# Optimization experiments

Measured on AMD Instinct MI355X. Metric: run time of the kernel, lower is better.

The kernel has to match this reference:

```python
import jax, jax.numpy as jnp
import numpy as np

D_MODEL = 1024
N_HEADS = 16
D_K = 64
D_V = 64
B = 2
S = 2048
NEG = -1e9
EPS = 1e-5  # torch nn.LayerNorm default


def setup_inputs() -> dict:
    key = jax.random.key(0)
    ks = jax.random.split(key, 8)
    inp = {
        "input_Q": jax.random.normal(ks[0], (B, S, D_MODEL), jnp.float32),
        "input_K": jax.random.normal(ks[1], (B, S, D_MODEL), jnp.float32),
        "input_V": jax.random.normal(ks[2], (B, S, D_MODEL), jnp.float32),
        "attn_mask": jax.random.randint(ks[3], (B, S, S), 0, 2).astype(bool),
        # torch nn.Linear weights are [out_features, in_features]; scale like default init
        "W_Q": jax.random.normal(ks[4], (N_HEADS * D_K, D_MODEL), jnp.float32) * (1.0 / np.sqrt(D_MODEL)),
        "W_K": jax.random.normal(ks[5], (N_HEADS * D_K, D_MODEL), jnp.float32) * (1.0 / np.sqrt(D_MODEL)),
        "W_V": jax.random.normal(ks[6], (N_HEADS * D_V, D_MODEL), jnp.float32) * (1.0 / np.sqrt(D_MODEL)),
        "W_fc": jax.random.normal(ks[7], (D_MODEL, N_HEADS * D_V), jnp.float32) * (1.0 / np.sqrt(N_HEADS * D_V)),
    }
    return inp


def _layernorm(x):
    # fresh nn.LayerNorm(d_model): weight=1, bias=0
    mu = jnp.mean(x, axis=-1, keepdims=True)
    var = jnp.mean(jnp.square(x - mu), axis=-1, keepdims=True)
    return (x - mu) * jax.lax.rsqrt(var + EPS)


def reference(input_Q, input_K, input_V, attn_mask, W_Q, W_K, W_V, W_fc):
    residual = input_Q
    # projections: x @ W.T, then split heads -> [B, H, S, d]
    def split_heads(x, d):
        return x.reshape(B, S, N_HEADS, d).transpose(0, 2, 1, 3)

    Q = split_heads(input_Q @ W_Q.T, D_K)
    K = split_heads(input_K @ W_K.T, D_K)
    V = split_heads(input_V @ W_V.T, D_V)

    scores = jnp.einsum("bhqd,bhkd->bhqk", Q, K) / np.sqrt(D_K).astype(np.float32)
    scores = jnp.where(attn_mask[:, None, :, :], NEG, scores)
    attn = jax.nn.softmax(scores, axis=-1)
    context = jnp.einsum("bhqk,bhkd->bhqd", attn, V)  # [B,H,S,Dv]
    context = context.transpose(0, 2, 1, 3).reshape(B, S, N_HEADS * D_V)
    output = context @ W_fc.T
    return _layernorm(output + residual), attn
```

## Files before the change

kernel.cpp:

```cpp
#include <hip/hip_runtime.h>

#define NB 2
#define SS 2048
#define DMODEL 1024
#define NH 16
#define DHEAD 64
#define QSCALE 0.1803368867f

typedef __bf16 bf16;
typedef bf16 bf16x8 __attribute__((ext_vector_type(8)));
typedef float f32x4 __attribute__((ext_vector_type(4)));
typedef unsigned char u8;

static __device__ __forceinline__ f32x4 mfma_16x16x32(bf16x8 a, bf16x8 b, f32x4 c) {
    return __builtin_amdgcn_mfma_f32_16x16x32_bf16(a, b, c, 0, 0, 0);
}

static __device__ __forceinline__ float fast_exp2(float x) {
#if __has_builtin(__builtin_amdgcn_exp2f)
    return __builtin_amdgcn_exp2f(x);
#else
    return __expf(x * 0.6931471805599453f);
#endif
}

static __device__ __forceinline__ bf16x8 cvt8(float4 u, float4 v) {
    bf16x8 r;
    r[0]=(bf16)u.x; r[1]=(bf16)u.y; r[2]=(bf16)u.z; r[3]=(bf16)u.w;
    r[4]=(bf16)v.x; r[5]=(bf16)v.y; r[6]=(bf16)v.z; r[7]=(bf16)v.w;
    return r;
}

__global__ __launch_bounds__(256) void pack_mask(const int* __restrict__ m,
                                                 u8* __restrict__ mb, int n4)
{
    const int i = blockIdx.x * blockDim.x + threadIdx.x;
    if (i < n4) {
        const int4 v = ((const int4*)m)[i];
        uchar4 o;
        o.x = (u8)v.x; o.y = (u8)v.y; o.z = (u8)v.z; o.w = (u8)v.w;
        ((uchar4*)mb)[i] = o;
    }
}

__global__ __launch_bounds__(256) void cvt_pair(const float* __restrict__ s0, bf16* __restrict__ d0, int n0_8,
                                                const float* __restrict__ s1, bf16* __restrict__ d1, int n1_8)
{
    const int i = blockIdx.x * blockDim.x + threadIdx.x;
    if (i < n0_8) {
        float4 u = ((const float4*)s0)[(size_t)i * 2];
        float4 v = ((const float4*)s0)[(size_t)i * 2 + 1];
        ((bf16x8*)d0)[i] = cvt8(u, v);
    } else if (i < n0_8 + n1_8) {
        const int j = i - n0_8;
        float4 u = ((const float4*)s1)[(size_t)j * 2];
        float4 v = ((const float4*)s1)[(size_t)j * 2 + 1];
        ((bf16x8*)d1)[j] = cvt8(u, v);
    }
}

__global__ __launch_bounds__(256) void gemm_bt(const bf16* __restrict__ A,
                                               const bf16* __restrict__ W,
                                               void* __restrict__ out, int mode,
                                               float scale)
{
    __shared__ bf16 As[128][40];
    __shared__ bf16 Ws[128][40];

    const int t  = threadIdx.x;
    const int wv = t >> 6, ln = t & 63, lo = ln & 15, qd = ln >> 4;
    const int wm = wv >> 1, wn = wv & 1;

    const int flat = blockIdx.x;
    const int swz  = ((flat & 7) << 5) + (flat >> 3);
    const int m0   = (swz >> 3) << 7;
    const int n0   = (swz & 7) << 7;

    const int srow = t >> 2, scol = (t & 3) << 3;
    const bf16* ap = A + (size_t)(m0 + srow) * DMODEL + scol;
    const bf16* wp = W + (size_t)(n0 + srow) * DMODEL + scol;

    f32x4 acc[4][4];
    #pragma unroll
    for (int i = 0; i < 4; ++i)
        #pragma unroll
        for (int j = 0; j < 4; ++j) acc[i][j] = (f32x4){0.f,0.f,0.f,0.f};

    bf16x8 a0 = *(const bf16x8*)ap;
    bf16x8 a1 = *(const bf16x8*)(ap + (size_t)64 * DMODEL);
    bf16x8 w0 = *(const bf16x8*)wp;
    bf16x8 w1 = *(const bf16x8*)(wp + (size_t)64 * DMODEL);

    for (int k0 = 0; k0 < DMODEL; k0 += 32) {
        __syncthreads();
        *(bf16x8*)&As[srow][scol]      = a0;
        *(bf16x8*)&As[64 + srow][scol] = a1;
        *(bf16x8*)&Ws[srow][scol]      = w0;
        *(bf16x8*)&Ws[64 + srow][scol] = w1;
        if (k0 + 32 < DMODEL) {
            a0 = *(const bf16x8*)(ap + k0 + 32);
            a1 = *(const bf16x8*)(ap + (size_t)64 * DMODEL + k0 + 32);
            w0 = *(const bf16x8*)(wp + k0 + 32);
            w1 = *(const bf16x8*)(wp + (size_t)64 * DMODEL + k0 + 32);
        }
        __syncthreads();
        bf16x8 af[4], wf[4];
        #pragma unroll
        for (int i = 0; i < 4; ++i)
            af[i] = *(const bf16x8*)&As[(wm << 6) + (i << 4) + lo][qd << 3];
        #pragma unroll
        for (int j = 0; j < 4; ++j)
            wf[j] = *(const bf16x8*)&Ws[(wn << 6) + (j << 4) + lo][qd << 3];
        #pragma unroll
        for (int i = 0; i < 4; ++i)
            #pragma unroll
            for (int j = 0; j < 4; ++j)
                acc[i][j] = mfma_16x16x32(af[i], wf[j], acc[i][j]);
    }

    #pragma unroll
    for (int i = 0; i < 4; ++i) {
        #pragma unroll
        for (int j = 0; j < 4; ++j) {
            #pragma unroll
            for (int r = 0; r < 4; ++r) {
                const int m = m0 + (wm << 6) + (i << 4) + (qd << 2) + r;
                const int n = n0 + (wn << 6) + (j << 4) + lo;
                const float v = acc[i][j][r] * scale;
                if (mode == 0) {
                    ((bf16*)out)[(size_t)m * DMODEL + n] = (bf16)v;
                } else if (mode == 1) {
                    ((bf16*)out)[((size_t)(m >> 11) * 1024 + n) * SS + (m & (SS - 1))] = (bf16)v;
                } else {
                    ((float*)out)[(size_t)m * DMODEL + n] = v;
                }
            }
        }
    }
}

__global__ __launch_bounds__(256) void attn_fused(const bf16* __restrict__ Qp,
                                                  const bf16* __restrict__ Kp,
                                                  const bf16* __restrict__ Vt,
                                                  const u8* __restrict__ mb,
                                                  float* __restrict__ attn_out,
                                                  bf16* __restrict__ ctxb)
{
    __shared__ bf16 Ks[2][32][72];
    __shared__ bf16 Pb[4][16][40];

    const int t  = threadIdx.x;
    const int wv = t >> 6, ln = t & 63, lo = ln & 15, qd = ln >> 4;

    const int flat = blockIdx.x;
    const int swz  = ((flat & 7) << 7) + (flat >> 3);
    const int q0 = (swz & 31) << 6;
    const int h  = (swz >> 5) & 15;
    const int b  = swz >> 9;
    const int bh = b * NH + h;

    const bf16* qsrc = Qp + (size_t)(b * SS + q0 + (wv << 4) + lo) * DMODEL + h * DHEAD + (qd << 3);
    const bf16x8 qa0 = *(const bf16x8*)qsrc;
    const bf16x8 qa1 = *(const bf16x8*)(qsrc + 32);

    const int srow = t >> 3, scol = (t & 7) << 3;
    const bf16* kbase = Kp + (size_t)(b * SS + srow) * DMODEL + h * DHEAD + scol;

    const u8* mrp[4];
    #pragma unroll
    for (int r = 0; r < 4; ++r)
        mrp[r] = mb + ((size_t)b * SS + q0 + (wv << 4) + (qd << 2) + r) * SS;

    const bf16* vbase = Vt + ((size_t)bh * DHEAD + lo) * SS + (qd << 3);

    f32x4 o[4];
    float lr[4] = {0.f, 0.f, 0.f, 0.f};
    #pragma unroll
    for (int j = 0; j < 4; ++j) o[j] = (f32x4){0.f,0.f,0.f,0.f};

    bf16x8 kreg = *(const bf16x8*)kbase;
    *(bf16x8*)&Ks[0][srow][scol] = kreg;
    kreg = *(const bf16x8*)(kbase + (size_t)32 * DMODEL);
    __syncthreads();

    for (int c = 0; c < 64; ++c) {
        if (c < 63) {
            *(bf16x8*)&Ks[(c + 1) & 1][srow][scol] = kreg;
            if (c < 62) kreg = *(const bf16x8*)(kbase + (size_t)(c + 2) * 32 * DMODEL);
        }
        const bf16 (*kb)[72] = Ks[c & 1];
        bf16x8 k00 = *(const bf16x8*)&kb[lo][qd << 3];
        bf16x8 k01 = *(const bf16x8*)&kb[lo][32 + (qd << 3)];
        bf16x8 k10 = *(const bf16x8*)&kb[16 + lo][qd << 3];
        bf16x8 k11 = *(const bf16x8*)&kb[16 + lo][32 + (qd << 3)];
        f32x4 s0 = (f32x4){0.f,0.f,0.f,0.f};
        s0 = mfma_16x16x32(qa0, k00, s0);
        s0 = mfma_16x16x32(qa1, k01, s0);
        f32x4 s1 = (f32x4){0.f,0.f,0.f,0.f};
        s1 = mfma_16x16x32(qa0, k10, s1);
        s1 = mfma_16x16x32(qa1, k11, s1);
        const int kc0 = c << 5;
        #pragma unroll
        for (int r = 0; r < 4; ++r) {
            const float e0 = mrp[r][kc0 + lo]      ? 0.f : fast_exp2(s0[r]);
            const float e1 = mrp[r][kc0 + 16 + lo] ? 0.f : fast_exp2(s1[r]);
            lr[r] += e0 + e1;
            Pb[wv][(qd << 2) + r][lo]      = (bf16)e0;
            Pb[wv][(qd << 2) + r][16 + lo] = (bf16)e1;
        }
        bf16x8 pa = *(const bf16x8*)&Pb[wv][lo][qd << 3];
        #pragma unroll
        for (int j = 0; j < 4; ++j) {
            bf16x8 vb = *(const bf16x8*)(vbase + (size_t)(j << 4) * SS + kc0);
            o[j] = mfma_16x16x32(pa, vb, o[j]);
        }
        __syncthreads();
    }

    #pragma unroll
    for (int r = 0; r < 4; ++r) {
        #pragma unroll
        for (int d = 1; d < 16; d <<= 1) lr[r] += __shfl_xor(lr[r], d);
    }
    float Li[4];
    #pragma unroll
    for (int r = 0; r < 4; ++r) Li[r] = 1.f / lr[r];

    #pragma unroll
    for (int j = 0; j < 4; ++j) {
        #pragma unroll
        for (int r = 0; r < 4; ++r) {
            ctxb[(size_t)(b * SS + q0 + (wv << 4) + (qd << 2) + r) * DMODEL
                 + h * DHEAD + (j << 4) + lo] = (bf16)(o[j][r] * Li[r]);
        }
    }

    kreg = *(const bf16x8*)kbase;
    *(bf16x8*)&Ks[0][srow][scol] = kreg;
    kreg = *(const bf16x8*)(kbase + (size_t)32 * DMODEL);
    __syncthreads();

    float* aout = attn_out + ((size_t)bh * SS + q0 + (wv << 4) + (qd << 2)) * SS;

    for (int c = 0; c < 64; ++c) {
        if (c < 63) {
            *(bf16x8*)&Ks[(c + 1) & 1][srow][scol] = kreg;
            if (c < 62) kreg = *(const bf16x8*)(kbase + (size_t)(c + 2) * 32 * DMODEL);
        }
        const bf16 (*kb)[72] = Ks[c & 1];
        bf16x8 k00 = *(const bf16x8*)&kb[lo][qd << 3];
        bf16x8 k01 = *(const bf16x8*)&kb[lo][32 + (qd << 3)];
        bf16x8 k10 = *(const bf16x8*)&kb[16 + lo][qd << 3];
        bf16x8 k11 = *(const bf16x8*)&kb[16 + lo][32 + (qd << 3)];
        f32x4 s0 = (f32x4){0.f,0.f,0.f,0.f};
        s0 = mfma_16x16x32(qa0, k00, s0);
        s0 = mfma_16x16x32(qa1, k01, s0);
        f32x4 s1 = (f32x4){0.f,0.f,0.f,0.f};
        s1 = mfma_16x16x32(qa0, k10, s1);
        s1 = mfma_16x16x32(qa1, k11, s1);
        const int kc0 = c << 5;
        #pragma unroll
        for (int r = 0; r < 4; ++r) {
            const float p0 = mrp[r][kc0 + lo]      ? 0.f : fast_exp2(s0[r]) * Li[r];
            const float p1 = mrp[r][kc0 + 16 + lo] ? 0.f : fast_exp2(s1[r]) * Li[r];
            aout[(size_t)r * SS + kc0 + lo]      = p0;
            aout[(size_t)r * SS + kc0 + 16 + lo] = p1;
        }
        __syncthreads();
    }
}

__global__ __launch_bounds__(256) void ln_resid(const float* __restrict__ O,
                                                const float* __restrict__ resid,
                                                float* __restrict__ out)
{
    const int row = blockIdx.x;
    const int t = threadIdx.x;
    const size_t base = (size_t)row * DMODEL + ((size_t)t << 2);
    const float4 o  = *(const float4*)(O + base);
    const float4 rs = *(const float4*)(resid + base);
    const float x0 = o.x + rs.x, x1 = o.y + rs.y, x2 = o.z + rs.z, x3 = o.w + rs.w;
    float s  = x0 + x1 + x2 + x3;
    float ss = x0*x0 + x1*x1 + x2*x2 + x3*x3;
    #pragma unroll
    for (int d = 32; d > 0; d >>= 1) {
        s  += __shfl_xor(s, d);
        ss += __shfl_xor(ss, d);
    }
    __shared__ float ws1[4], ws2[4];
    if ((t & 63) == 0) { ws1[t >> 6] = s; ws2[t >> 6] = ss; }
    __syncthreads();
    s  = ws1[0] + ws1[1] + ws1[2] + ws1[3];
    ss = ws2[0] + ws2[1] + ws2[2] + ws2[3];
    const float mu  = s * (1.f / DMODEL);
    const float var = ss * (1.f / DMODEL) - mu * mu;
    const float inv = rsqrtf(var + 1e-5f);
    float4 y;
    y.x = (x0 - mu) * inv; y.y = (x1 - mu) * inv;
    y.z = (x2 - mu) * inv; y.w = (x3 - mu) * inv;
    *(float4*)(out + base) = y;
}

extern "C" void kernel_launch(void* const* d_in, const int* in_sizes, int n_in,
                              void* d_out, int out_size, void* d_ws, size_t ws_size,
                              hipStream_t stream)
{
    const float* inQ = (const float*)d_in[0];
    const float* inK = (const float*)d_in[1];
    const float* inV = (const float*)d_in[2];
    const int*   msk = (const int*)d_in[3];
    const float* WQ  = (const float*)d_in[4];
    const float* WK  = (const float*)d_in[5];
    const float* WV  = (const float*)d_in[6];
    const float* Wfc = (const float*)d_in[7];

    float* out_ln   = (float*)d_out;
    float* out_attn = out_ln + (size_t)NB * SS * DMODEL;

    char* w = (char*)d_ws;
    const size_t MB = 1024 * 1024;
    bf16*  Qp   = (bf16*)(w);
    bf16*  Kp   = (bf16*)(w + 8  * MB);
    bf16*  Vt   = (bf16*)(w + 16 * MB);
    bf16*  ctxb = (bf16*)(w + 24 * MB);
    bf16*  Abf  = (bf16*)(w + 32 * MB);
    u8*    mkb  = (u8*)  (w + 40 * MB);
    bf16*  Wbf  = (bf16*)(w + 48 * MB);
    float* Obuf = (float*)(w + 32 * MB);

    dim3 blk(256);

    const int n4 = (NB * SS * SS) / 4;
    pack_mask<<<dim3(n4 / 256), blk, 0, stream>>>(msk, mkb, n4);

    const int nIn8 = (NB * SS * DMODEL) / 8;
    const int nW8  = (DMODEL * DMODEL) / 8;
    const int cvtBoth = (nIn8 + nW8 + 255) / 256;
    const int cvtW    = (nW8 + 255) / 256;

    cvt_pair<<<dim3(cvtBoth), blk, 0, stream>>>(inQ, Abf, nIn8, WQ, Wbf, nW8);
    gemm_bt<<<dim3(256), blk, 0, stream>>>(Abf, Wbf, (void*)Qp, 0, QSCALE);

    cvt_pair<<<dim3(cvtBoth), blk, 0, stream>>>(inK, Abf, nIn8, WK, Wbf, nW8);
    gemm_bt<<<dim3(256), blk, 0, stream>>>(Abf, Wbf, (void*)Kp, 0, 1.0f);

    cvt_pair<<<dim3(cvtBoth), blk, 0, stream>>>(inV, Abf, nIn8, WV, Wbf, nW8);
    gemm_bt<<<dim3(256), blk, 0, stream>>>(Abf, Wbf, (void*)Vt, 1, 1.0f);

    attn_fused<<<dim3(SS / 64 * NH * NB), blk, 0, stream>>>(Qp, Kp, Vt, mkb, out_attn, ctxb);

    cvt_pair<<<dim3(cvtW), blk, 0, stream>>>(Wfc, Wbf, nW8, (const float*)0, (bf16*)0, 0);
    gemm_bt<<<dim3(256), blk, 0, stream>>>(ctxb, Wbf, (void*)Obuf, 2, 1.0f);

    ln_resid<<<dim3(NB * SS), blk, 0, stream>>>(Obuf, inQ, out_ln);
}
```

Measured before the change: 966.5 us.

## Bit-pack mask, stage V in LDS, shrink GEMM tiles and add occupancy hints

The mask is packed to one bit per element with a wave ballot instead of one byte per element, which cuts mask traffic in both attention passes. The attention kernel now stages V tiles in double-buffered shared memory instead of reading them straight from global memory. The GEMM tile shrinks from 128x128 to 64x128 with twice the blocks, and launch_bounds occupancy hints are added. Risks include extra LDS pressure, and the smaller GEMM tile reuses each loaded tile less.

```diff
diff --git a/kernel.cpp b/kernel.cpp
--- a/kernel.cpp
+++ b/kernel.cpp
@@ -11,6 +11,8 @@
 typedef bf16 bf16x8 __attribute__((ext_vector_type(8)));
 typedef float f32x4 __attribute__((ext_vector_type(4)));
 typedef unsigned char u8;
+typedef unsigned int u32;
+typedef unsigned long long u64;
 
 static __device__ __forceinline__ f32x4 mfma_16x16x32(bf16x8 a, bf16x8 b, f32x4 c) {
     return __builtin_amdgcn_mfma_f32_16x16x32_bf16(a, b, c, 0, 0, 0);
@@ -31,16 +33,13 @@
     return r;
 }
 
-__global__ __launch_bounds__(256) void pack_mask(const int* __restrict__ m,
-                                                 u8* __restrict__ mb, int n4)
-{
-    const int i = blockIdx.x * blockDim.x + threadIdx.x;
-    if (i < n4) {
-        const int4 v = ((const int4*)m)[i];
-        uchar4 o;
-        o.x = (u8)v.x; o.y = (u8)v.y; o.z = (u8)v.z; o.w = (u8)v.w;
-        ((uchar4*)mb)[i] = o;
-    }
+__global__ __launch_bounds__(256) void pack_mask_bits(const int* __restrict__ m,
+                                                      u64* __restrict__ bits, int n)
+{
+    const int i = blockIdx.x * 256 + threadIdx.x;
+    const int v = (i < n) ? m[i] : 0;
+    const u64 bal = __ballot(v != 0);
+    if ((threadIdx.x & 63) == 0) bits[i >> 6] = bal;
 }
 
 __global__ __launch_bounds__(256) void cvt_pair(const float* __restrict__ s0, bf16* __restrict__ d0, int n0_8,
@@ -59,12 +58,12 @@
     }
 }
 
-__global__ __launch_bounds__(256) void gemm_bt(const bf16* __restrict__ A,
-                                               const bf16* __restrict__ W,
-                                               void* __restrict__ out, int mode,
-                                               float scale)
-{
-    __shared__ bf16 As[128][40];
+__global__ __launch_bounds__(256, 2) void gemm_bt(const bf16* __restrict__ A,
+                                                  const bf16* __restrict__ W,
+                                                  void* __restrict__ out, int mode,
+                                                  float scale)
+{
+    __shared__ bf16 As[64][40];
     __shared__ bf16 Ws[128][40];
 
     const int t  = threadIdx.x;
@@ -72,59 +71,56 @@
     const int wm = wv >> 1, wn = wv & 1;
 
     const int flat = blockIdx.x;
-    const int swz  = ((flat & 7) << 5) + (flat >> 3);
-    const int m0   = (swz >> 3) << 7;
-    const int n0   = (swz & 7) << 7;
-
-    const int srow = t >> 2, scol = (t & 3) << 3;
-    const bf16* ap = A + (size_t)(m0 + srow) * DMODEL + scol;
-    const bf16* wp = W + (size_t)(n0 + srow) * DMODEL + scol;
-
-    f32x4 acc[4][4];
-    #pragma unroll
-    for (int i = 0; i < 4; ++i)
+    const int m0   = (flat >> 3) << 6;
+    const int n0   = (flat & 7) << 7;
+
+    const int srowA = t >> 2, scolA = (t & 3) << 3;
+    const int srowW = t >> 1, scolW = (t & 1) << 4;
+    const bf16* ap = A + (size_t)(m0 + srowA) * DMODEL + scolA;
+    const bf16* wp = W + (size_t)(n0 + srowW) * DMODEL + scolW;
+
+    f32x4 acc[2][4];
+    #pragma unroll
+    for (int i = 0; i < 2; ++i)
         #pragma unroll
         for (int j = 0; j < 4; ++j) acc[i][j] = (f32x4){0.f,0.f,0.f,0.f};
 
     bf16x8 a0 = *(const bf16x8*)ap;
-    bf16x8 a1 = *(const bf16x8*)(ap + (size_t)64 * DMODEL);
     bf16x8 w0 = *(const bf16x8*)wp;
-    bf16x8 w1 = *(const bf16x8*)(wp + (size_t)64 * DMODEL);
+    bf16x8 w1 = *(const bf16x8*)(wp + 8);
 
     for (int k0 = 0; k0 < DMODEL; k0 += 32) {
         __syncthreads();
-        *(bf16x8*)&As[srow][scol]      = a0;
-        *(bf16x8*)&As[64 + srow][scol] = a1;
-        *(bf16x8*)&Ws[srow][scol]      = w0;
-        *(bf16x8*)&Ws[64 + srow][scol] = w1;
+        *(bf16x8*)&As[srowA][scolA]     = a0;
+        *(bf16x8*)&Ws[srowW][scolW]     = w0;
+        *(bf16x8*)&Ws[srowW][scolW + 8] = w1;
         if (k0 + 32 < DMODEL) {
             a0 = *(const bf16x8*)(ap + k0 + 32);
-            a1 = *(const bf16x8*)(ap + (size_t)64 * DMODEL + k0 + 32);
             w0 = *(const bf16x8*)(wp + k0 + 32);
-            w1 = *(const bf16x8*)(wp + (size_t)64 * DMODEL + k0 + 32);
+            w1 = *(const bf16x8*)(wp + k0 + 40);
         }
         __syncthreads();
-        bf16x8 af[4], wf[4];
-        #pragma unroll
-        for (int i = 0; i < 4; ++i)
-            af[i] = *(const bf16x8*)&As[(wm << 6) + (i << 4) + lo][qd << 3];
+        bf16x8 af[2], wf[4];
+        #pragma unroll
+        for (int i = 0; i < 2; ++i)
+            af[i] = *(const bf16x8*)&As[(wm << 5) + (i << 4) + lo][qd << 3];
         #pragma unroll
         for (int j = 0; j < 4; ++j)
             wf[j] = *(const bf16x8*)&Ws[(wn << 6) + (j << 4) + lo][qd << 3];
         #pragma unroll
-        for (int i = 0; i < 4; ++i)
+        for (int i = 0; i < 2; ++i)
             #pragma unroll
             for (int j = 0; j < 4; ++j)
                 acc[i][j] = mfma_16x16x32(af[i], wf[j], acc[i][j]);
     }
 
     #pragma unroll
-    for (int i = 0; i < 4; ++i) {
+    for (int i = 0; i < 2; ++i) {
         #pragma unroll
         for (int j = 0; j < 4; ++j) {
             #pragma unroll
             for (int r = 0; r < 4; ++r) {
-                const int m = m0 + (wm << 6) + (i << 4) + (qd << 2) + r;
+                const int m = m0 + (wm << 5) + (i << 4) + (qd << 2) + r;
                 const int n = n0 + (wn << 6) + (j << 4) + lo;
                 const float v = acc[i][j][r] * scale;
                 if (mode == 0) {
@@ -139,14 +135,15 @@
     }
 }
 
-__global__ __launch_bounds__(256) void attn_fused(const bf16* __restrict__ Qp,
-                                                  const bf16* __restrict__ Kp,
-                                                  const bf16* __restrict__ Vt,
-                                                  const u8* __restrict__ mb,
-                                                  float* __restrict__ attn_out,
-                                                  bf16* __restrict__ ctxb)
+__global__ __launch_bounds__(256, 4) void attn_fused(const bf16* __restrict__ Qp,
+                                                     const bf16* __restrict__ Kp,
+                                                     const bf16* __restrict__ Vt,
+                                                     const u32* __restrict__ mbits,
+                                                     float* __restrict__ attn_out,
+                                                     bf16* __restrict__ ctxb)
 {
     __shared__ bf16 Ks[2][32][72];
+    __shared__ bf16 Vs[2][64][40];
     __shared__ bf16 Pb[4][16][40];
 
     const int t  = threadIdx.x;
@@ -163,15 +160,12 @@
     const bf16x8 qa0 = *(const bf16x8*)qsrc;
     const bf16x8 qa1 = *(const bf16x8*)(qsrc + 32);
 
-    const int srow = t >> 3, scol = (t & 7) << 3;
-    const bf16* kbase = Kp + (size_t)(b * SS + srow) * DMODEL + h * DHEAD + scol;
-
-    const u8* mrp[4];
-    #pragma unroll
-    for (int r = 0; r < 4; ++r)
-        mrp[r] = mb + ((size_t)b * SS + q0 + (wv << 4) + (qd << 2) + r) * SS;
-
-    const bf16* vbase = Vt + ((size_t)bh * DHEAD + lo) * SS + (qd << 3);
+    const int srowK = t >> 3, scolK = (t & 7) << 3;
+    const bf16* kbase = Kp + (size_t)(b * SS + srowK) * DMODEL + h * DHEAD + scolK;
+    const int srowV = t >> 2, scolV = (t & 3) << 3;
+    const bf16* vstb = Vt + ((size_t)bh * DHEAD + srowV) * SS + scolV;
+
+    const int mrow0 = b * SS + q0 + (wv << 4) + (qd << 2);
 
     f32x4 o[4];
     float lr[4] = {0.f, 0.f, 0.f, 0.f};
@@ -179,13 +173,80 @@
     for (int j = 0; j < 4; ++j) o[j] = (f32x4){0.f,0.f,0.f,0.f};
 
     bf16x8 kreg = *(const bf16x8*)kbase;
-    *(bf16x8*)&Ks[0][srow][scol] = kreg;
+    bf16x8 vreg = *(const bf16x8*)vstb;
+    *(bf16x8*)&Ks[0][srowK][scolK] = kreg;
+    *(bf16x8*)&Vs[0][srowV][scolV] = vreg;
+    kreg = *(const bf16x8*)(kbase + (size_t)32 * DMODEL);
+    vreg = *(const bf16x8*)(vstb + 32);
+    __syncthreads();
+
+    for (int c = 0; c < 64; ++c) {
+        if (c < 63) {
+            *(bf16x8*)&Ks[(c + 1) & 1][srowK][scolK] = kreg;
+            *(bf16x8*)&Vs[(c + 1) & 1][srowV][scolV] = vreg;
+            if (c < 62) {
+                kreg = *(const bf16x8*)(kbase + (size_t)(c + 2) * 32 * DMODEL);
+                vreg = *(const bf16x8*)(vstb + (c + 2) * 32);
+            }
+        }
+        const bf16 (*kb)[72] = Ks[c & 1];
+        bf16x8 k00 = *(const bf16x8*)&kb[lo][qd << 3];
+        bf16x8 k01 = *(const bf16x8*)&kb[lo][32 + (qd << 3)];
+        bf16x8 k10 = *(const bf16x8*)&kb[16 + lo][qd << 3];
+        bf16x8 k11 = *(const bf16x8*)&kb[16 + lo][32 + (qd << 3)];
+        f32x4 s0 = (f32x4){0.f,0.f,0.f,0.f};
+        s0 = mfma_16x16x32(qa0, k00, s0);
+        s0 = mfma_16x16x32(qa1, k01, s0);
+        f32x4 s1 = (f32x4){0.f,0.f,0.f,0.f};
+        s1 = mfma_16x16x32(qa0, k10, s1);
+        s1 = mfma_16x16x32(qa1, k11, s1);
+        #pragma unroll
+        for (int r = 0; r < 4; ++r) {
+            const u32 wrd = mbits[(mrow0 + r) * 64 + c];
+            const float e0 = ((wrd >> lo) & 1u)        ? 0.f : fast_exp2(s0[r]);
+            const float e1 = ((wrd >> (16 + lo)) & 1u) ? 0.f : fast_exp2(s1[r]);
+            lr[r] += e0 + e1;
+            Pb[wv][(qd << 2) + r][lo]      = (bf16)e0;
+            Pb[wv][(qd << 2) + r][16 + lo] = (bf16)e1;
+        }
+        bf16x8 pa = *(const bf16x8*)&Pb[wv][lo][qd << 3];
+        const bf16 (*vsc)[40] = Vs[c & 1];
+        #pragma unroll
+        for (int j = 0; j < 4; ++j) {
+            bf16x8 vf = *(const bf16x8*)&vsc[(j << 4) + lo][qd << 3];
+            o[j] = mfma_16x16x32(pa, vf, o[j]);
+        }
+        __syncthreads();
+    }
+
+    #pragma unroll
+    for (int r = 0; r < 4; ++r) {
+        #pragma unroll
+        for (int d = 1; d < 16; d <<= 1) lr[r] += __shfl_xor(lr[r], d);
+    }
+    float Li[4];
+    #pragma unroll
+    for (int r = 0; r < 4; ++r) Li[r] = 1.f / lr[r];
+
+    #pragma unroll
+    for (int j = 0; j < 4; ++j) {
+        #pragma unroll
+        for (int r = 0; r < 4; ++r) {
+            ctxb[(size_t)(b * SS + q0 + (wv << 4) + (qd << 2) + r) * DMODEL
+                 + h * DHEAD + (j << 4) + lo] = (bf16)(o[j][r] * Li[r]);
+        }
+    }
+
+    kreg = *(const bf16x8*)kbase;
+    *(bf16x8*)&Ks[0][srowK][scolK] = kreg;
     kreg = *(const bf16x8*)(kbase + (size_t)32 * DMODEL);
     __syncthreads();
 
+    float* aout = attn_out + ((size_t)bh * SS + q0 + (wv << 4) + (qd << 2)) * SS;
+
     for (int c = 0; c < 64; ++c) {
         if (c < 63) {
-            *(bf16x8*)&Ks[(c + 1) & 1][srow][scol] = kreg;
+            *(bf16x8*)&Ks[(c + 1) & 1][srowK][scolK] = kreg;
             if (c < 62) kreg = *(const bf16x8*)(kbase + (size_t)(c + 2) * 32 * DMODEL);
         }
         const bf16 (*kb)[72] = Ks[c & 1];
@@ -202,67 +263,9 @@
         const int kc0 = c << 5;
         #pragma unroll
         for (int r = 0; r < 4; ++r) {
-            const float e0 = mrp[r][kc0 + lo]      ? 0.f : fast_exp2(s0[r]);
-            const float e1 = mrp[r][kc0 + 16 + lo] ? 0.f : fast_exp2(s1[r]);
-            lr[r] += e0 + e1;
-            Pb[wv][(qd << 2) + r][lo]      = (bf16)e0;
-            Pb[wv][(qd << 2) + r][16 + lo] = (bf16)e1;
-        }
-        bf16x8 pa = *(const bf16x8*)&Pb[wv][lo][qd << 3];
-        #pragma unroll
-        for (int j = 0; j < 4; ++j) {
-            bf16x8 vb = *(const bf16x8*)(vbase + (size_t)(j << 4) * SS + kc0);
-            o[j] = mfma_16x16x32(pa, vb, o[j]);
-        }
-        __syncthreads();
-    }
-
-    #pragma unroll
-    for (int r = 0; r < 4; ++r) {
-        #pragma unroll
-        for (int d = 1; d < 16; d <<= 1) lr[r] += __shfl_xor(lr[r], d);
-    }
-    float Li[4];
-    #pragma unroll
-    for (int r = 0; r < 4; ++r) Li[r] = 1.f / lr[r];
-
-    #pragma unroll
-    for (int j = 0; j < 4; ++j) {
-        #pragma unroll
-        for (int r = 0; r < 4; ++r) {
-            ctxb[(size_t)(b * SS + q0 + (wv << 4) + (qd << 2) + r) * DMODEL
-                 + h * DHEAD + (j << 4) + lo] = (bf16)(o[j][r] * Li[r]);
-        }
-    }
-
-    kreg = *(const bf16x8*)kbase;
-    *(bf16x8*)&Ks[0][srow][scol] = kreg;
-    kreg = *(const bf16x8*)(kbase + (size_t)32 * DMODEL);
-    __syncthreads();
-
-    float* aout = attn_out + ((size_t)bh * SS + q0 + (wv << 4) + (qd << 2)) * SS;
-
-    for (int c = 0; c < 64; ++c) {
-        if (c < 63) {
-            *(bf16x8*)&Ks[(c + 1) & 1][srow][scol] = kreg;
-            if (c < 62) kreg = *(const bf16x8*)(kbase + (size_t)(c + 2) * 32 * DMODEL);
-        }
-        const bf16 (*kb)[72] = Ks[c & 1];
-        bf16x8 k00 = *(const bf16x8*)&kb[lo][qd << 3];
-        bf16x8 k01 = *(const bf16x8*)&kb[lo][32 + (qd << 3)];
-        bf16x8 k10 = *(const bf16x8*)&kb[16 + lo][qd << 3];
-        bf16x8 k11 = *(const bf16x8*)&kb[16 + lo][32 + (qd << 3)];
-        f32x4 s0 = (f32x4){0.f,0.f,0.f,0.f};
-        s0 = mfma_16x16x32(qa0, k00, s0);
-        s0 = mfma_16x16x32(qa1, k01, s0);
-        f32x4 s1 = (f32x4){0.f,0.f,0.f,0.f};
-        s1 = mfma_16x16x32(qa0, k10, s1);
-        s1 = mfma_16x16x32(qa1, k11, s1);
-        const int kc0 = c << 5;
-        #pragma unroll
-        for (int r = 0; r < 4; ++r) {
-            const float p0 = mrp[r][kc0 + lo]      ? 0.f : fast_exp2(s0[r]) * Li[r];
-            const float p1 = mrp[r][kc0 + 16 + lo] ? 0.f : fast_exp2(s1[r]) * Li[r];
+            const u32 wrd = mbits[(mrow0 + r) * 64 + c];
+            const float p0 = ((wrd >> lo) & 1u)        ? 0.f : fast_exp2(s0[r]) * Li[r];
+            const float p1 = ((wrd >> (16 + lo)) & 1u) ? 0.f : fast_exp2(s1[r]) * Li[r];
             aout[(size_t)r * SS + kc0 + lo]      = p0;
             aout[(size_t)r * SS + kc0 + 16 + lo] = p1;
         }
@@ -319,19 +322,19 @@
 
     char* w = (char*)d_ws;
     const size_t MB = 1024 * 1024;
-    bf16*  Qp   = (bf16*)(w);
-    bf16*  Kp   = (bf16*)(w + 8  * MB);
-    bf16*  Vt   = (bf16*)(w + 16 * MB);
-    bf16*  ctxb = (bf16*)(w + 24 * MB);
-    bf16*  Abf  = (bf16*)(w + 32 * MB);
-    u8*    mkb  = (u8*)  (w + 40 * MB);
-    bf16*  Wbf  = (bf16*)(w + 48 * MB);
-    float* Obuf = (float*)(w + 32 * MB);
+    bf16*  Qp    = (bf16*)(w);
+    bf16*  Kp    = (bf16*)(w + 8  * MB);
+    bf16*  Vt    = (bf16*)(w + 16 * MB);
+    bf16*  ctxb  = (bf16*)(w + 24 * MB);
+    bf16*  Abf   = (bf16*)(w + 32 * MB);
+    bf16*  Wbf   = (bf16*)(w + 40 * MB);
+    u64*   mbits = (u64*) (w + 42 * MB);
+    float* Obuf  = (float*)(w);
 
     dim3 blk(256);
 
-    const int n4 = (NB * SS * SS) / 4;
-    pack_mask<<<dim3(n4 / 256), blk, 0, stream>>>(msk, mkb, n4);
+    const int nMask = NB * SS * SS;
+    pack_mask_bits<<<dim3(nMask / 256), blk, 0, stream>>>(msk, mbits, nMask);
 
     const int nIn8 = (NB * SS * DMODEL) / 8;
     const int nW8  = (DMODEL * DMODEL) / 8;
@@ -339,18 +342,20 @@
     const int cvtW    = (nW8 + 255) / 256;
 
     cvt_pair<<<dim3(cvtBoth), blk, 0, stream>>>(inQ, Abf, nIn8, WQ, Wbf, nW8);
-    gemm_bt<<<dim3(256), blk, 0, stream>>>(Abf, Wbf, (void*)Qp, 0, QSCALE);
+    gemm_bt<<<dim3(512), blk, 0, stream>>>(Abf, Wbf, (void*)Qp, 0, QSCALE);
 
     cvt_pair<<<dim3(cvtBoth), blk, 0, stream>>>(inK, Abf, nIn8, WK, Wbf, nW8);
-    gemm_bt<<<dim3(256), blk, 0, stream>>>(Abf, Wbf, (void*)Kp, 0, 1.0f);
+    gemm_bt<<<dim3(512), blk, 0, stream>>>(Abf, Wbf, (void*)Kp, 0, 1.0f);
 
     cvt_pair<<<dim3(cvtBoth), blk, 0, stream>>>(inV, Abf, nIn8, WV, Wbf, nW8);
-    gemm_bt<<<dim3(256), blk, 0, stream>>>(Abf, Wbf, (void*)Vt, 1, 1.0f);
-
-    attn_fused<<<dim3(SS / 64 * NH * NB), blk, 0, stream>>>(Qp, Kp, Vt, mkb, out_attn, ctxb);
+    gemm_bt<<<dim3(512), blk, 0, stream>>>(Abf, Wbf, (void*)Vt, 1, 1.0f);
 
     cvt_pair<<<dim3(cvtW), blk, 0, stream>>>(Wfc, Wbf, nW8, (const float*)0, (bf16*)0, 0);
-    gemm_bt<<<dim3(256), blk, 0, stream>>>(ctxb, Wbf, (void*)Obuf, 2, 1.0f);
+
+    attn_fused<<<dim3(SS / 64 * NH * NB), blk, 0, stream>>>(Qp, Kp, Vt, (const u32*)mbits,
+                                                            out_attn, ctxb);
+
+    gemm_bt<<<dim3(512), blk, 0, stream>>>(ctxb, Wbf, (void*)Obuf, 2, 1.0f);
 
     ln_resid<<<dim3(NB * SS), blk, 0, stream>>>(Obuf, inQ, out_ln);
 }
```

After: 831.1 us. -14.0%, faster.
